# Kernel optimization log

Measured on AMD Instinct MI355X. Metric: run time of the kernel, lower is better.

The kernel has to match this reference:

```python
import jax, jax.numpy as jnp
import numpy as np

NSLICES = 4
HID = 512
IN_FEAT = 342   # input_shape - 1 (last column is phase)
OUT = 311
BATCH = 256


def cubic(y0, y1, y2, y3, mu):
    # Catmull-Rom cubic interpolation, as in the original PFNN code
    return (
        (-0.5 * y0 + 1.5 * y1 - 1.5 * y2 + 0.5 * y3) * mu * mu * mu
        + (y0 - 2.5 * y1 + 2.0 * y2 - 0.5 * y3) * mu * mu
        + (-0.5 * y0 + 0.5 * y2) * mu
        + y1
    )


def setup_inputs() -> dict:
    key = jax.random.key(0)
    ks = jax.random.split(key, 7)
    x = jax.random.uniform(ks[0], (BATCH, IN_FEAT + 1), dtype=jnp.float32)
    s = 0.02
    W0 = jax.random.normal(ks[1], (NSLICES, HID, IN_FEAT), dtype=jnp.float32) * s
    b0 = jax.random.normal(ks[2], (NSLICES, HID), dtype=jnp.float32) * s
    W1 = jax.random.normal(ks[3], (NSLICES, HID, HID), dtype=jnp.float32) * s
    b1 = jax.random.normal(ks[4], (NSLICES, HID), dtype=jnp.float32) * s
    W2 = jax.random.normal(ks[5], (NSLICES, OUT, HID), dtype=jnp.float32) * s
    b2 = jax.random.normal(ks[6], (NSLICES, OUT), dtype=jnp.float32) * s
    return {"x": x, "W0": W0, "b0": b0, "W1": W1, "b1": b1, "W2": W2, "b2": b2}


def reference(x, W0, b0, W1, b1, W2, b2):
    phase = x[:, -1]                       # [B]
    pscale = NSLICES * phase
    mu = jnp.mod(pscale, 1.0)              # [B]
    i1 = jnp.floor(pscale).astype(jnp.int32) % NSLICES
    i0 = (i1 - 1) % NSLICES
    i2 = (i1 + 1) % NSLICES
    i3 = (i1 + 2) % NSLICES
    muW = mu[:, None, None]                # broadcast over (out, in)
    mub = mu[:, None]

    Wb0 = cubic(W0[i0], W0[i1], W0[i2], W0[i3], muW)   # [B, 512, 342]
    bb0 = cubic(b0[i0], b0[i1], b0[i2], b0[i3], mub)   # [B, 512]
    Wb1 = cubic(W1[i0], W1[i1], W1[i2], W1[i3], muW)   # [B, 512, 512]
    bb1 = cubic(b1[i0], b1[i1], b1[i2], b1[i3], mub)
    Wb2 = cubic(W2[i0], W2[i1], W2[i2], W2[i3], muW)   # [B, 311, 512]
    bb2 = cubic(b2[i0], b2[i1], b2[i2], b2[i3], mub)

    h = x[:, :-1]                                       # [B, 342]
    h = jax.nn.elu(jnp.einsum('boi,bi->bo', Wb0, h) + bb0)
    h = jax.nn.elu(jnp.einsum('boi,bi->bo', Wb1, h) + bb1)
    out = jnp.einsum('boi,bi->bo', Wb2, h) + bb2        # [B, 311]
    return out
```

## Files before the change

### kernel.cpp

```cpp
#include <hip/hip_runtime.h>
#include <math.h>

#define NSLICES 4
#define HID 512
#define IN_FEAT 342
#define OUTD 311
#define BATCH 256
#define KP0 352
#define MP2 320
#define XROW (IN_FEAT + 1)

typedef unsigned short u16;
typedef short bf16x8 __attribute__((ext_vector_type(8)));
typedef float f32x4 __attribute__((ext_vector_type(4)));

__device__ __forceinline__ u16 f2bf_rne(float v) {
    unsigned int x = __float_as_uint(v);
    unsigned int r = (x + 0x7fffu + ((x >> 16) & 1u)) >> 16;
    return (u16)r;
}
__device__ __forceinline__ float bf2f(u16 u) {
    return __uint_as_float(((unsigned int)u) << 16);
}

#define C0 (4 * 512 * 44)
#define C1 (4 * 512 * 64)
#define C2 (4 * 320 * 64)
#define CX (256 * 44)
#define PREP_TOT (C0 + C1 + C2 + CX + 256)

union U8 { u16 u[8]; uint4 v; };

__global__ __launch_bounds__(256) void prep_all(
    const float* __restrict__ x,
    const float* __restrict__ W0, const float* __restrict__ W1, const float* __restrict__ W2,
    u16* __restrict__ whi0, u16* __restrict__ wlo0,
    u16* __restrict__ whi1, u16* __restrict__ wlo1,
    u16* __restrict__ whi2, u16* __restrict__ wlo2,
    u16* __restrict__ h0hi, u16* __restrict__ h0lo,
    float* __restrict__ dcoef)
{
    int i = blockIdx.x * 256 + threadIdx.x;
    if (i >= PREP_TOT) return;

    if (i >= C0 + C1 + C2 + CX) {
        int b = i - (C0 + C1 + C2 + CX);
        float ps = 4.f * x[(size_t)b * XROW + IN_FEAT];
        float fl = floorf(ps);
        float mu = ps - fl;
        int i1 = ((int)fl) & 3;
        float mu2 = mu * mu, mu3 = mu2 * mu;
        float c0 = -0.5f * mu3 + mu2 - 0.5f * mu;
        float c1 = 1.5f * mu3 - 2.5f * mu2 + 1.0f;
        float c2 = -1.5f * mu3 + 2.0f * mu2 + 0.5f * mu;
        float c3 = 0.5f * mu3 - 0.5f * mu2;
        float d[4];
        d[(i1 + 3) & 3] = c0;
        d[i1]           = c1;
        d[(i1 + 1) & 3] = c2;
        d[(i1 + 2) & 3] = c3;
        *reinterpret_cast<float4*>(dcoef + b * 4) = make_float4(d[0], d[1], d[2], d[3]);
        return;
    }

    float src[8];
    u16* dhi; u16* dlo; size_t doff;
    if (i < C0) {
        int row = i / 44, c = i - row * 44;
        int k = c * 8;
#pragma unroll
        for (int j = 0; j < 8; j++) {
            int kk = k + j;
            src[j] = (kk < IN_FEAT) ? W0[(size_t)row * IN_FEAT + kk] : 0.f;
        }
        dhi = whi0; dlo = wlo0; doff = (size_t)row * KP0 + k;
    } else if (i < C0 + C1) {
        int l = i - C0;
        int row = l >> 6, c = l & 63;
        int k = c * 8;
        const float* p = W1 + (size_t)row * HID + k;
#pragma unroll
        for (int j = 0; j < 8; j++) src[j] = p[j];
        dhi = whi1; dlo = wlo1; doff = (size_t)row * HID + k;
    } else if (i < C0 + C1 + C2) {
        int l = i - C0 - C1;
        int row = l >> 6, c = l & 63;
        int k = c * 8;
        int s = row / 320, o = row - s * 320;
        if (o < OUTD) {
            const float* p = W2 + ((size_t)s * OUTD + o) * HID + k;
#pragma unroll
            for (int j = 0; j < 8; j++) src[j] = p[j];
        } else {
#pragma unroll
            for (int j = 0; j < 8; j++) src[j] = 0.f;
        }
        dhi = whi2; dlo = wlo2; doff = (size_t)row * HID + k;
    } else {
        int l = i - C0 - C1 - C2;
        int b = l / 44, c = l - b * 44;
        int k = c * 8;
#pragma unroll
        for (int j = 0; j < 8; j++) {
            int kk = k + j;
            src[j] = (kk < IN_FEAT) ? x[(size_t)b * XROW + kk] : 0.f;
        }
        dhi = h0hi; dlo = h0lo; doff = (size_t)b * KP0 + k;
    }

    U8 hi, lo;
#pragma unroll
    for (int j = 0; j < 8; j++) {
        u16 h = f2bf_rne(src[j]);
        hi.u[j] = h;
        lo.u[j] = f2bf_rne(src[j] - bf2f(h));
    }
    *reinterpret_cast<uint4*>(dhi + doff) = hi.v;
    *reinterpret_cast<uint4*>(dlo + doff) = lo.v;
}

template<int KP, int KLDS, int FINAL>
__global__ __launch_bounds__(256, 2) void layer_fused2(
    const u16* __restrict__ Whi, const u16* __restrict__ Wlo,
    const u16* __restrict__ Hhi, const u16* __restrict__ Hlo,
    const float* __restrict__ bias, const float* __restrict__ dcoef,
    int Mp, int M,
    u16* __restrict__ Ohi, u16* __restrict__ Olo, float* __restrict__ out)
{
    __shared__ __align__(16) u16 sHhi[16 * KLDS];
    __shared__ __align__(16) u16 sHlo[16 * KLDS];
    __shared__ float sAcc[4][16][17];

    const int tid = (int)threadIdx.x;
    const int b0 = blockIdx.x * 16;
    const int o0 = blockIdx.y * 16;

    constexpr int CH = KP / 8;
    for (int idx = tid; idx < 16 * CH; idx += 256) {
        int r = idx / CH, c = idx - r * CH;
        size_t g = (size_t)(b0 + r) * KP + c * 8;
        *reinterpret_cast<uint4*>(&sHhi[r * KLDS + c * 8]) =
            *reinterpret_cast<const uint4*>(Hhi + g);
        *reinterpret_cast<uint4*>(&sHlo[r * KLDS + c * 8]) =
            *reinterpret_cast<const uint4*>(Hlo + g);
    }
    __syncthreads();

    const int lane = tid & 63;
    const int s  = tid >> 6;
    const int m  = lane & 15;
    const int q  = lane >> 4;

    const u16* hp_hi = &sHhi[m * KLDS + q * 8];
    const u16* hp_lo = &sHlo[m * KLDS + q * 8];
    const size_t wrow = ((size_t)s * Mp + o0 + m) * KP + q * 8;
    const u16* wp_hi = Whi + wrow;
    const u16* wp_lo = Wlo + wrow;

    f32x4 a0 = {0.f, 0.f, 0.f, 0.f};
    f32x4 a1 = {0.f, 0.f, 0.f, 0.f};
    f32x4 a2 = {0.f, 0.f, 0.f, 0.f};
#pragma unroll
    for (int c = 0; c < KP / 32; ++c) {
        bf16x8 ah = *reinterpret_cast<const bf16x8*>(wp_hi + c * 32);
        bf16x8 al = *reinterpret_cast<const bf16x8*>(wp_lo + c * 32);
        bf16x8 bh = *reinterpret_cast<const bf16x8*>(hp_hi + c * 32);
        bf16x8 b_l = *reinterpret_cast<const bf16x8*>(hp_lo + c * 32);
        a0 = __builtin_amdgcn_mfma_f32_16x16x32_bf16(ah, bh, a0, 0, 0, 0);
        a1 = __builtin_amdgcn_mfma_f32_16x16x32_bf16(ah, b_l, a1, 0, 0, 0);
        a2 = __builtin_amdgcn_mfma_f32_16x16x32_bf16(al, bh, a2, 0, 0, 0);
    }
    f32x4 sum = a0 + a1 + a2;

    const float ds = dcoef[(size_t)(b0 + m) * 4 + s];
#pragma unroll
    for (int r = 0; r < 4; ++r) {
        int o = o0 + q * 4 + r;
        float bb = (o < M) ? bias[(size_t)s * M + o] : 0.f;
        sAcc[s][q * 4 + r][m] = ds * (sum[r] + bb);
    }
    __syncthreads();

    const int o_l = tid & 15;
    const int b_l = tid >> 4;
    float v = sAcc[0][o_l][b_l] + sAcc[1][o_l][b_l]
            + sAcc[2][o_l][b_l] + sAcc[3][o_l][b_l];
    const int o = o0 + o_l;
    const int b = b0 + b_l;
    if (!FINAL) {
        float e = (v > 0.f) ? v : expm1f(v);
        u16 h = f2bf_rne(e);
        Ohi[(size_t)b * M + o] = h;
        Olo[(size_t)b * M + o] = f2bf_rne(e - bf2f(h));
    } else {
        if (o < M) out[(size_t)b * M + o] = v;
    }
}

extern "C" void kernel_launch(void* const* d_in, const int* in_sizes, int n_in,
                              void* d_out, int out_size, void* d_ws, size_t ws_size,
                              hipStream_t stream) {
    const float* x  = (const float*)d_in[0];
    const float* W0 = (const float*)d_in[1];
    const float* b0 = (const float*)d_in[2];
    const float* W1 = (const float*)d_in[3];
    const float* b1 = (const float*)d_in[4];
    const float* W2 = (const float*)d_in[5];
    const float* b2 = (const float*)d_in[6];
    float* out = (float*)d_out;

    char* p = (char*)d_ws;
    auto alloc = [&](size_t bytes) { char* r = p; p += (bytes + 255) & ~(size_t)255; return r; };

    float* dcoef = (float*)alloc(BATCH * 4 * sizeof(float));
    u16* whi0 = (u16*)alloc((size_t)4 * HID * KP0 * 2);
    u16* wlo0 = (u16*)alloc((size_t)4 * HID * KP0 * 2);
    u16* whi1 = (u16*)alloc((size_t)4 * HID * HID * 2);
    u16* wlo1 = (u16*)alloc((size_t)4 * HID * HID * 2);
    u16* whi2 = (u16*)alloc((size_t)4 * MP2 * HID * 2);
    u16* wlo2 = (u16*)alloc((size_t)4 * MP2 * HID * 2);
    u16* h0hi = (u16*)alloc((size_t)BATCH * KP0 * 2);
    u16* h0lo = (u16*)alloc((size_t)BATCH * KP0 * 2);
    u16* hahi = (u16*)alloc((size_t)BATCH * HID * 2);
    u16* halo = (u16*)alloc((size_t)BATCH * HID * 2);
    u16* hbhi = (u16*)alloc((size_t)BATCH * HID * 2);
    u16* hblo = (u16*)alloc((size_t)BATCH * HID * 2);

    prep_all<<<dim3((PREP_TOT + 255) / 256), 256, 0, stream>>>(
        x, W0, W1, W2, whi0, wlo0, whi1, wlo1, whi2, wlo2, h0hi, h0lo, dcoef);

    layer_fused2<KP0, KP0 + 8, 0><<<dim3(BATCH / 16, HID / 16), 256, 0, stream>>>(
        whi0, wlo0, h0hi, h0lo, b0, dcoef, HID, HID, hahi, halo, nullptr);

    layer_fused2<HID, HID + 8, 0><<<dim3(BATCH / 16, HID / 16), 256, 0, stream>>>(
        whi1, wlo1, hahi, halo, b1, dcoef, HID, HID, hbhi, hblo, nullptr);

    layer_fused2<HID, HID + 8, 1><<<dim3(BATCH / 16, MP2 / 16), 256, 0, stream>>>(
        whi2, wlo2, hbhi, hblo, b2, dcoef, MP2, OUTD, nullptr, nullptr, out);
}
```

Before: 102.2 us.

## Merge prep and three layers into one cooperative persistent kernel with grid syncs

Replaces four separate launches with a single cooperative kernel of 256 blocks that runs weight and activation splitting, then the three layers, with grid-wide syncs between phases. Each block now computes a 32-batch by 16-output tile, staging activations through LDS in chunks of 8 k-steps, so every weight fragment load feeds two MFMA batch tiles. This removes launch gaps and halves weight reloads per batch. In exchange it pays grid-sync overhead, gives less parallelism per layer (256 blocks, and only 160 active in the last layer), and adds extra block syncs for the chunked LDS staging.

```diff
diff --git a/kernel.cpp b/kernel.cpp
--- a/kernel.cpp
+++ b/kernel.cpp
@@ -1,7 +1,9 @@
 #include <hip/hip_runtime.h>
+#include <hip/hip_cooperative_groups.h>
 #include <math.h>
 
-#define NSLICES 4
+namespace cg = cooperative_groups;
+
 #define HID 512
 #define IN_FEAT 342
 #define OUTD 311
@@ -9,6 +11,7 @@
 #define KP0 352
 #define MP2 320
 #define XROW (IN_FEAT + 1)
+#define LSTRIDE 264
 
 typedef unsigned short u16;
 typedef short bf16x8 __attribute__((ext_vector_type(8)));
@@ -31,210 +34,237 @@
 
 union U8 { u16 u[8]; uint4 v; };
 
-__global__ __launch_bounds__(256) void prep_all(
-    const float* __restrict__ x,
-    const float* __restrict__ W0, const float* __restrict__ W1, const float* __restrict__ W2,
-    u16* __restrict__ whi0, u16* __restrict__ wlo0,
-    u16* __restrict__ whi1, u16* __restrict__ wlo1,
-    u16* __restrict__ whi2, u16* __restrict__ wlo2,
-    u16* __restrict__ h0hi, u16* __restrict__ h0lo,
-    float* __restrict__ dcoef)
+union SharedU {
+    u16 h[2][32 * LSTRIDE];
+    float acc[4][32][17];
+};
+
+struct Params {
+    const float *x, *W0, *b0, *W1, *b1, *W2, *b2;
+    float* out;
+    u16 *whi0, *wlo0, *whi1, *wlo1, *whi2, *wlo2;
+    u16 *h0hi, *h0lo, *hahi, *halo, *hbhi, *hblo;
+    float* dcoef;
+};
+
+__device__ __forceinline__ void layer_phase(
+    SharedU& sm,
+    const u16* __restrict__ Whi, const u16* __restrict__ Wlo, int wstride, int Mp,
+    const u16* __restrict__ Hhi, const u16* __restrict__ Hlo, int hstride, int nch,
+    const float* __restrict__ bias, const float* __restrict__ dcoef, int Mb,
+    int OT, int FINAL,
+    u16* __restrict__ Ohi, u16* __restrict__ Olo, float* __restrict__ outp)
 {
-    int i = blockIdx.x * 256 + threadIdx.x;
-    if (i >= PREP_TOT) return;
-
-    if (i >= C0 + C1 + C2 + CX) {
-        int b = i - (C0 + C1 + C2 + CX);
-        float ps = 4.f * x[(size_t)b * XROW + IN_FEAT];
-        float fl = floorf(ps);
-        float mu = ps - fl;
-        int i1 = ((int)fl) & 3;
-        float mu2 = mu * mu, mu3 = mu2 * mu;
-        float c0 = -0.5f * mu3 + mu2 - 0.5f * mu;
-        float c1 = 1.5f * mu3 - 2.5f * mu2 + 1.0f;
-        float c2 = -1.5f * mu3 + 2.0f * mu2 + 0.5f * mu;
-        float c3 = 0.5f * mu3 - 0.5f * mu2;
-        float d[4];
-        d[(i1 + 3) & 3] = c0;
-        d[i1]           = c1;
-        d[(i1 + 1) & 3] = c2;
-        d[(i1 + 2) & 3] = c3;
-        *reinterpret_cast<float4*>(dcoef + b * 4) = make_float4(d[0], d[1], d[2], d[3]);
-        return;
-    }
-
-    float src[8];
-    u16* dhi; u16* dlo; size_t doff;
-    if (i < C0) {
-        int row = i / 44, c = i - row * 44;
-        int k = c * 8;
-#pragma unroll
-        for (int j = 0; j < 8; j++) {
-            int kk = k + j;
-            src[j] = (kk < IN_FEAT) ? W0[(size_t)row * IN_FEAT + kk] : 0.f;
-        }
-        dhi = whi0; dlo = wlo0; doff = (size_t)row * KP0 + k;
-    } else if (i < C0 + C1) {
-        int l = i - C0;
-        int row = l >> 6, c = l & 63;
-        int k = c * 8;
-        const float* p = W1 + (size_t)row * HID + k;
-#pragma unroll
-        for (int j = 0; j < 8; j++) src[j] = p[j];
-        dhi = whi1; dlo = wlo1; doff = (size_t)row * HID + k;
-    } else if (i < C0 + C1 + C2) {
-        int l = i - C0 - C1;
-        int row = l >> 6, c = l & 63;
-        int k = c * 8;
-        int s = row / 320, o = row - s * 320;
-        if (o < OUTD) {
-            const float* p = W2 + ((size_t)s * OUTD + o) * HID + k;
-#pragma unroll
-            for (int j = 0; j < 8; j++) src[j] = p[j];
-        } else {
-#pragma unroll
-            for (int j = 0; j < 8; j++) src[j] = 0.f;
-        }
-        dhi = whi2; dlo = wlo2; doff = (size_t)row * HID + k;
-    } else {
-        int l = i - C0 - C1 - C2;
-        int b = l / 44, c = l - b * 44;
-        int k = c * 8;
-#pragma unroll
-        for (int j = 0; j < 8; j++) {
-            int kk = k + j;
-            src[j] = (kk < IN_FEAT) ? x[(size_t)b * XROW + kk] : 0.f;
-        }
-        dhi = h0hi; dlo = h0lo; doff = (size_t)b * KP0 + k;
-    }
-
-    U8 hi, lo;
-#pragma unroll
-    for (int j = 0; j < 8; j++) {
-        u16 h = f2bf_rne(src[j]);
-        hi.u[j] = h;
-        lo.u[j] = f2bf_rne(src[j] - bf2f(h));
-    }
-    *reinterpret_cast<uint4*>(dhi + doff) = hi.v;
-    *reinterpret_cast<uint4*>(dlo + doff) = lo.v;
-}
-
-template<int KP, int KLDS, int FINAL>
-__global__ __launch_bounds__(256, 2) void layer_fused2(
-    const u16* __restrict__ Whi, const u16* __restrict__ Wlo,
-    const u16* __restrict__ Hhi, const u16* __restrict__ Hlo,
-    const float* __restrict__ bias, const float* __restrict__ dcoef,
-    int Mp, int M,
-    u16* __restrict__ Ohi, u16* __restrict__ Olo, float* __restrict__ out)
-{
-    __shared__ __align__(16) u16 sHhi[16 * KLDS];
-    __shared__ __align__(16) u16 sHlo[16 * KLDS];
-    __shared__ float sAcc[4][16][17];
-
+    const int unit = (int)blockIdx.x;
+    if (unit >= OT * 8) return;
+    int ot, bq;
+    if (OT == 32) { ot = unit & 31; bq = unit >> 5; }
+    else          { ot = unit % OT; bq = unit / OT; }
+    const int o0 = ot * 16;
+    const int b0 = bq * 32;
     const int tid = (int)threadIdx.x;
-    const int b0 = blockIdx.x * 16;
-    const int o0 = blockIdx.y * 16;
-
-    constexpr int CH = KP / 8;
-    for (int idx = tid; idx < 16 * CH; idx += 256) {
-        int r = idx / CH, c = idx - r * CH;
-        size_t g = (size_t)(b0 + r) * KP + c * 8;
-        *reinterpret_cast<uint4*>(&sHhi[r * KLDS + c * 8]) =
-            *reinterpret_cast<const uint4*>(Hhi + g);
-        *reinterpret_cast<uint4*>(&sHlo[r * KLDS + c * 8]) =
-            *reinterpret_cast<const uint4*>(Hlo + g);
+    const int lane = tid & 63;
+    const int s = tid >> 6;
+    const int m = lane & 15;
+    const int q = lane >> 4;
+
+    f32x4 a0[2], a1[2], a2[2];
+#pragma unroll
+    for (int bt = 0; bt < 2; ++bt) {
+        a0[bt] = (f32x4){0.f, 0.f, 0.f, 0.f};
+        a1[bt] = (f32x4){0.f, 0.f, 0.f, 0.f};
+        a2[bt] = (f32x4){0.f, 0.f, 0.f, 0.f};
+    }
+
+    const u16* wph = Whi + ((size_t)s * Mp + o0 + m) * wstride + q * 8;
+    const u16* wpl = Wlo + ((size_t)s * Mp + o0 + m) * wstride + q * 8;
+
+    for (int c0 = 0; c0 < nch; c0 += 8) {
+        const int rc = (nch - c0 < 8) ? (nch - c0) : 8;
+        __syncthreads();
+        const int tot = 32 * rc * 4;
+        for (int idx = tid; idx < tot; idx += 256) {
+            int r = idx / (rc * 4);
+            int c = idx - r * (rc * 4);
+            size_t g = (size_t)(b0 + r) * hstride + c0 * 32 + c * 8;
+            *reinterpret_cast<uint4*>(&sm.h[0][r * LSTRIDE + c * 8]) =
+                *reinterpret_cast<const uint4*>(Hhi + g);
+            *reinterpret_cast<uint4*>(&sm.h[1][r * LSTRIDE + c * 8]) =
+                *reinterpret_cast<const uint4*>(Hlo + g);
+        }
+        __syncthreads();
+        for (int cc = 0; cc < rc; ++cc) {
+            bf16x8 ah = *reinterpret_cast<const bf16x8*>(wph + (size_t)(c0 + cc) * 32);
+            bf16x8 al = *reinterpret_cast<const bf16x8*>(wpl + (size_t)(c0 + cc) * 32);
+#pragma unroll
+            for (int bt = 0; bt < 2; ++bt) {
+                const u16* base = &sm.h[0][(bt * 16 + m) * LSTRIDE + cc * 32 + q * 8];
+                bf16x8 bh = *reinterpret_cast<const bf16x8*>(base);
+                bf16x8 bl = *reinterpret_cast<const bf16x8*>(base + 32 * LSTRIDE);
+                a0[bt] = __builtin_amdgcn_mfma_f32_16x16x32_bf16(ah, bh, a0[bt], 0, 0, 0);
+                a1[bt] = __builtin_amdgcn_mfma_f32_16x16x32_bf16(ah, bl, a1[bt], 0, 0, 0);
+                a2[bt] = __builtin_amdgcn_mfma_f32_16x16x32_bf16(al, bh, a2[bt], 0, 0, 0);
+            }
+        }
     }
     __syncthreads();
 
-    const int lane = tid & 63;
-    const int s  = tid >> 6;
-    const int m  = lane & 15;
-    const int q  = lane >> 4;
-
-    const u16* hp_hi = &sHhi[m * KLDS + q * 8];
-    const u16* hp_lo = &sHlo[m * KLDS + q * 8];
-    const size_t wrow = ((size_t)s * Mp + o0 + m) * KP + q * 8;
-    const u16* wp_hi = Whi + wrow;
-    const u16* wp_lo = Wlo + wrow;
-
-    f32x4 a0 = {0.f, 0.f, 0.f, 0.f};
-    f32x4 a1 = {0.f, 0.f, 0.f, 0.f};
-    f32x4 a2 = {0.f, 0.f, 0.f, 0.f};
-#pragma unroll
-    for (int c = 0; c < KP / 32; ++c) {
-        bf16x8 ah = *reinterpret_cast<const bf16x8*>(wp_hi + c * 32);
-        bf16x8 al = *reinterpret_cast<const bf16x8*>(wp_lo + c * 32);
-        bf16x8 bh = *reinterpret_cast<const bf16x8*>(hp_hi + c * 32);
-        bf16x8 b_l = *reinterpret_cast<const bf16x8*>(hp_lo + c * 32);
-        a0 = __builtin_amdgcn_mfma_f32_16x16x32_bf16(ah, bh, a0, 0, 0, 0);
-        a1 = __builtin_amdgcn_mfma_f32_16x16x32_bf16(ah, b_l, a1, 0, 0, 0);
-        a2 = __builtin_amdgcn_mfma_f32_16x16x32_bf16(al, bh, a2, 0, 0, 0);
-    }
-    f32x4 sum = a0 + a1 + a2;
-
-    const float ds = dcoef[(size_t)(b0 + m) * 4 + s];
+    float bb[4];
 #pragma unroll
     for (int r = 0; r < 4; ++r) {
         int o = o0 + q * 4 + r;
-        float bb = (o < M) ? bias[(size_t)s * M + o] : 0.f;
-        sAcc[s][q * 4 + r][m] = ds * (sum[r] + bb);
+        bb[r] = (o < Mb) ? bias[(size_t)s * Mb + o] : 0.f;
+    }
+    const float ds0 = dcoef[(size_t)(b0 + m) * 4 + s];
+    const float ds1 = dcoef[(size_t)(b0 + 16 + m) * 4 + s];
+#pragma unroll
+    for (int bt = 0; bt < 2; ++bt) {
+        f32x4 sum = a0[bt] + a1[bt] + a2[bt];
+        const float dsv = bt ? ds1 : ds0;
+#pragma unroll
+        for (int r = 0; r < 4; ++r)
+            sm.acc[s][bt * 16 + m][q * 4 + r] = dsv * (sum[r] + bb[r]);
     }
     __syncthreads();
 
-    const int o_l = tid & 15;
-    const int b_l = tid >> 4;
-    float v = sAcc[0][o_l][b_l] + sAcc[1][o_l][b_l]
-            + sAcc[2][o_l][b_l] + sAcc[3][o_l][b_l];
-    const int o = o0 + o_l;
-    const int b = b0 + b_l;
-    if (!FINAL) {
-        float e = (v > 0.f) ? v : expm1f(v);
-        u16 h = f2bf_rne(e);
-        Ohi[(size_t)b * M + o] = h;
-        Olo[(size_t)b * M + o] = f2bf_rne(e - bf2f(h));
-    } else {
-        if (o < M) out[(size_t)b * M + o] = v;
-    }
+    for (int idx = tid; idx < 512; idx += 256) {
+        int b_l = idx >> 4, o_l = idx & 15;
+        float v = sm.acc[0][b_l][o_l] + sm.acc[1][b_l][o_l]
+                + sm.acc[2][b_l][o_l] + sm.acc[3][b_l][o_l];
+        int o = o0 + o_l, b = b0 + b_l;
+        if (!FINAL) {
+            float e = (v > 0.f) ? v : expm1f(v);
+            u16 h = f2bf_rne(e);
+            Ohi[(size_t)b * HID + o] = h;
+            Olo[(size_t)b * HID + o] = f2bf_rne(e - bf2f(h));
+        } else if (o < OUTD) {
+            outp[(size_t)b * OUTD + o] = v;
+        }
+    }
+}
+
+__global__ __launch_bounds__(256) void pfn_coop(Params p)
+{
+    __shared__ SharedU sm;
+    cg::grid_group grid = cg::this_grid();
+
+    for (int i = (int)blockIdx.x * 256 + (int)threadIdx.x; i < PREP_TOT; i += 256 * 256) {
+        if (i >= C0 + C1 + C2 + CX) {
+            int b = i - (C0 + C1 + C2 + CX);
+            float ps = 4.f * p.x[(size_t)b * XROW + IN_FEAT];
+            float fl = floorf(ps);
+            float mu = ps - fl;
+            int i1 = ((int)fl) & 3;
+            float mu2 = mu * mu, mu3 = mu2 * mu;
+            float c0 = -0.5f * mu3 + mu2 - 0.5f * mu;
+            float c1 = 1.5f * mu3 - 2.5f * mu2 + 1.0f;
+            float c2 = -1.5f * mu3 + 2.0f * mu2 + 0.5f * mu;
+            float c3 = 0.5f * mu3 - 0.5f * mu2;
+            float d[4];
+            d[(i1 + 3) & 3] = c0;
+            d[i1]           = c1;
+            d[(i1 + 1) & 3] = c2;
+            d[(i1 + 2) & 3] = c3;
+            *reinterpret_cast<float4*>(p.dcoef + b * 4) = make_float4(d[0], d[1], d[2], d[3]);
+            continue;
+        }
+        float src[8];
+        u16 *dhi, *dlo; size_t doff;
+        if (i < C0) {
+            int row = i / 44, c = i - row * 44;
+            int k = c * 8;
+#pragma unroll
+            for (int j = 0; j < 8; j++) {
+                int kk = k + j;
+                src[j] = (kk < IN_FEAT) ? p.W0[(size_t)row * IN_FEAT + kk] : 0.f;
+            }
+            dhi = p.whi0; dlo = p.wlo0; doff = (size_t)row * KP0 + k;
+        } else if (i < C0 + C1) {
+            int l = i - C0;
+            int row = l >> 6, c = l & 63;
+            int k = c * 8;
+            const float* sp = p.W1 + (size_t)row * HID + k;
+#pragma unroll
+            for (int j = 0; j < 8; j++) src[j] = sp[j];
+            dhi = p.whi1; dlo = p.wlo1; doff = (size_t)row * HID + k;
+        } else if (i < C0 + C1 + C2) {
+            int l = i - C0 - C1;
+            int row = l >> 6, c = l & 63;
+            int k = c * 8;
+            int s = row / 320, o = row - s * 320;
+            if (o < OUTD) {
+                const float* sp = p.W2 + ((size_t)s * OUTD + o) * HID + k;
+#pragma unroll
+                for (int j = 0; j < 8; j++) src[j] = sp[j];
+            } else {
+#pragma unroll
+                for (int j = 0; j < 8; j++) src[j] = 0.f;
+            }
+            dhi = p.whi2; dlo = p.wlo2; doff = (size_t)row * HID + k;
+        } else {
+            int l = i - C0 - C1 - C2;
+            int b = l / 44, c = l - b * 44;
+            int k = c * 8;
+#pragma unroll
+            for (int j = 0; j < 8; j++) {
+                int kk = k + j;
+                src[j] = (kk < IN_FEAT) ? p.x[(size_t)b * XROW + kk] : 0.f;
+            }
+            dhi = p.h0hi; dlo = p.h0lo; doff = (size_t)b * KP0 + k;
+        }
+        U8 hi, lo;
+#pragma unroll
+        for (int j = 0; j < 8; j++) {
+            u16 h = f2bf_rne(src[j]);
+            hi.u[j] = h;
+            lo.u[j] = f2bf_rne(src[j] - bf2f(h));
+        }
+        *reinterpret_cast<uint4*>(dhi + doff) = hi.v;
+        *reinterpret_cast<uint4*>(dlo + doff) = lo.v;
+    }
+
+    grid.sync();
+    layer_phase(sm, p.whi0, p.wlo0, KP0, HID, p.h0hi, p.h0lo, KP0, 11,
+                p.b0, p.dcoef, HID, 32, 0, p.hahi, p.halo, nullptr);
+    grid.sync();
+    layer_phase(sm, p.whi1, p.wlo1, HID, HID, p.hahi, p.halo, HID, 16,
+                p.b1, p.dcoef, HID, 32, 0, p.hbhi, p.hblo, nullptr);
+    grid.sync();
+    layer_phase(sm, p.whi2, p.wlo2, HID, MP2, p.hbhi, p.hblo, HID, 16,
+                p.b2, p.dcoef, OUTD, 20, 1, nullptr, nullptr, p.out);
 }
 
 extern "C" void kernel_launch(void* const* d_in, const int* in_sizes, int n_in,
                               void* d_out, int out_size, void* d_ws, size_t ws_size,
                               hipStream_t stream) {
-    const float* x  = (const float*)d_in[0];
-    const float* W0 = (const float*)d_in[1];
-    const float* b0 = (const float*)d_in[2];
-    const float* W1 = (const float*)d_in[3];
-    const float* b1 = (const float*)d_in[4];
-    const float* W2 = (const float*)d_in[5];
-    const float* b2 = (const float*)d_in[6];
-    float* out = (float*)d_out;
-
-    char* p = (char*)d_ws;
-    auto alloc = [&](size_t bytes) { char* r = p; p += (bytes + 255) & ~(size_t)255; return r; };
-
-    float* dcoef = (float*)alloc(BATCH * 4 * sizeof(float));
-    u16* whi0 = (u16*)alloc((size_t)4 * HID * KP0 * 2);
-    u16* wlo0 = (u16*)alloc((size_t)4 * HID * KP0 * 2);
-    u16* whi1 = (u16*)alloc((size_t)4 * HID * HID * 2);
-    u16* wlo1 = (u16*)alloc((size_t)4 * HID * HID * 2);
-    u16* whi2 = (u16*)alloc((size_t)4 * MP2 * HID * 2);
-    u16* wlo2 = (u16*)alloc((size_t)4 * MP2 * HID * 2);
-    u16* h0hi = (u16*)alloc((size_t)BATCH * KP0 * 2);
-    u16* h0lo = (u16*)alloc((size_t)BATCH * KP0 * 2);
-    u16* hahi = (u16*)alloc((size_t)BATCH * HID * 2);
-    u16* halo = (u16*)alloc((size_t)BATCH * HID * 2);
-    u16* hbhi = (u16*)alloc((size_t)BATCH * HID * 2);
-    u16* hblo = (u16*)alloc((size_t)BATCH * HID * 2);
-
-    prep_all<<<dim3((PREP_TOT + 255) / 256), 256, 0, stream>>>(
-        x, W0, W1, W2, whi0, wlo0, whi1, wlo1, whi2, wlo2, h0hi, h0lo, dcoef);
-
-    layer_fused2<KP0, KP0 + 8, 0><<<dim3(BATCH / 16, HID / 16), 256, 0, stream>>>(
-        whi0, wlo0, h0hi, h0lo, b0, dcoef, HID, HID, hahi, halo, nullptr);
-
-    layer_fused2<HID, HID + 8, 0><<<dim3(BATCH / 16, HID / 16), 256, 0, stream>>>(
-        whi1, wlo1, hahi, halo, b1, dcoef, HID, HID, hbhi, hblo, nullptr);
-
-    layer_fused2<HID, HID + 8, 1><<<dim3(BATCH / 16, MP2 / 16), 256, 0, stream>>>(
-        whi2, wlo2, hbhi, hblo, b2, dcoef, MP2, OUTD, nullptr, nullptr, out);
-}
+    char* pw = (char*)d_ws;
+    auto alloc = [&](size_t bytes) { char* r = pw; pw += (bytes + 255) & ~(size_t)255; return r; };
+
+    Params p;
+    p.x  = (const float*)d_in[0];
+    p.W0 = (const float*)d_in[1];
+    p.b0 = (const float*)d_in[2];
+    p.W1 = (const float*)d_in[3];
+    p.b1 = (const float*)d_in[4];
+    p.W2 = (const float*)d_in[5];
+    p.b2 = (const float*)d_in[6];
+    p.out = (float*)d_out;
+
+    p.dcoef = (float*)alloc(BATCH * 4 * sizeof(float));
+    p.whi0 = (u16*)alloc((size_t)4 * HID * KP0 * 2);
+    p.wlo0 = (u16*)alloc((size_t)4 * HID * KP0 * 2);
+    p.whi1 = (u16*)alloc((size_t)4 * HID * HID * 2);
+    p.wlo1 = (u16*)alloc((size_t)4 * HID * HID * 2);
+    p.whi2 = (u16*)alloc((size_t)4 * MP2 * HID * 2);
+    p.wlo2 = (u16*)alloc((size_t)4 * MP2 * HID * 2);
+    p.h0hi = (u16*)alloc((size_t)BATCH * KP0 * 2);
+    p.h0lo = (u16*)alloc((size_t)BATCH * KP0 * 2);
+    p.hahi = (u16*)alloc((size_t)BATCH * HID * 2);
+    p.halo = (u16*)alloc((size_t)BATCH * HID * 2);
+    p.hbhi = (u16*)alloc((size_t)BATCH * HID * 2);
+    p.hblo = (u16*)alloc((size_t)BATCH * HID * 2);
+
+    void* args[] = { &p };
+    hipLaunchCooperativeKernel(reinterpret_cast<const void*>(&pfn_coop),
+                               dim3(256), dim3(256), args, 0, stream);
+}
```

Result: slower. 214.8 us (+110.2%).

## Fuse weight bf16 split conversion into layer kernels, drop prep pass

Applied to the files above, without the earlier changes.

Removes the separate prep kernel that converted all weights and inputs into hi/lo bf16 arrays in workspace. Each layer kernel now reads fp32 weights directly and splits them into hi/lo bf16 in registers before the MFMAs. Layer 0 converts x in shared memory, and every kernel computes its own blend coefficients. This saves a launch and a write-then-read round trip of the converted weights. In exchange, each weight row is now read as fp32 (twice the bytes) by every batch tile and reconverted there, and shared memory is unioned between the activations and the accumulator.

```diff
diff --git a/kernel.cpp b/kernel.cpp
--- a/kernel.cpp
+++ b/kernel.cpp
@@ -1,14 +1,12 @@
 #include <hip/hip_runtime.h>
 #include <math.h>
 
-#define NSLICES 4
 #define HID 512
 #define IN_FEAT 342
 #define OUTD 311
 #define BATCH 256
+#define XROW (IN_FEAT + 1)
 #define KP0 352
-#define MP2 320
-#define XROW (IN_FEAT + 1)
 
 typedef unsigned short u16;
 typedef short bf16x8 __attribute__((ext_vector_type(8)));
@@ -23,29 +21,109 @@
     return __uint_as_float(((unsigned int)u) << 16);
 }
 
-#define C0 (4 * 512 * 44)
-#define C1 (4 * 512 * 64)
-#define C2 (4 * 320 * 64)
-#define CX (256 * 44)
-#define PREP_TOT (C0 + C1 + C2 + CX + 256)
+__device__ __forceinline__ void cvt8(const float* v, bf16x8& hi, bf16x8& lo) {
+#pragma unroll
+    for (int j = 0; j < 8; j++) {
+        unsigned int xu = __float_as_uint(v[j]);
+        unsigned int rnd = xu + 0x7fffu + ((xu >> 16) & 1u);
+        hi[j] = (short)(rnd >> 16);
+        float lof = v[j] - __uint_as_float(rnd & 0xffff0000u);
+        lo[j] = (short)(__float_as_uint(lof) >> 16);
+    }
+}
 
-union U8 { u16 u[8]; uint4 v; };
+template<int KCH, int KLDS, int FINAL, int L0>
+__global__ __launch_bounds__(256, 2) void layer_direct(
+    const float* __restrict__ W,
+    int Kw, int Mreal, int Mb,
+    const float* __restrict__ x,
+    const u16* __restrict__ Hhi, const u16* __restrict__ Hlo,
+    const float* __restrict__ bias,
+    u16* __restrict__ Ohi, u16* __restrict__ Olo, float* __restrict__ outp)
+{
+    union SharedU {
+        u16 h[2][16 * KLDS];
+        float acc[4][16][17];
+    };
+    __shared__ SharedU sm;
 
-__global__ __launch_bounds__(256) void prep_all(
-    const float* __restrict__ x,
-    const float* __restrict__ W0, const float* __restrict__ W1, const float* __restrict__ W2,
-    u16* __restrict__ whi0, u16* __restrict__ wlo0,
-    u16* __restrict__ whi1, u16* __restrict__ wlo1,
-    u16* __restrict__ whi2, u16* __restrict__ wlo2,
-    u16* __restrict__ h0hi, u16* __restrict__ h0lo,
-    float* __restrict__ dcoef)
-{
-    int i = blockIdx.x * 256 + threadIdx.x;
-    if (i >= PREP_TOT) return;
+    const int tid = (int)threadIdx.x;
+    const int b0 = (int)blockIdx.x * 16;
+    const int o0 = (int)blockIdx.y * 16;
 
-    if (i >= C0 + C1 + C2 + CX) {
-        int b = i - (C0 + C1 + C2 + CX);
-        float ps = 4.f * x[(size_t)b * XROW + IN_FEAT];
+    if (L0) {
+        for (int idx = tid; idx < 16 * KP0; idx += 256) {
+            int r = idx / KP0, k = idx - r * KP0;
+            float v = (k < IN_FEAT) ? x[(size_t)(b0 + r) * XROW + k] : 0.f;
+            u16 h = f2bf_rne(v);
+            sm.h[0][r * KLDS + k] = h;
+            sm.h[1][r * KLDS + k] = f2bf_rne(v - bf2f(h));
+        }
+    } else {
+        constexpr int CH = KCH * 4;
+        for (int idx = tid; idx < 16 * CH; idx += 256) {
+            int r = idx / CH, c = idx - r * CH;
+            size_t g = (size_t)(b0 + r) * HID + c * 8;
+            *reinterpret_cast<uint4*>(&sm.h[0][r * KLDS + c * 8]) =
+                *reinterpret_cast<const uint4*>(Hhi + g);
+            *reinterpret_cast<uint4*>(&sm.h[1][r * KLDS + c * 8]) =
+                *reinterpret_cast<const uint4*>(Hlo + g);
+        }
+    }
+    __syncthreads();
+
+    const int lane = tid & 63;
+    const int s = tid >> 6;
+    const int m = lane & 15;
+    const int q = lane >> 4;
+
+    int orow = o0 + m;
+    if (orow >= Mreal) orow = Mreal - 1;
+    const float* wr = W + ((size_t)s * Mreal + orow) * Kw;
+
+    const u16* hp = &sm.h[0][m * KLDS + q * 8];
+
+    f32x4 a0 = {0.f, 0.f, 0.f, 0.f};
+    f32x4 a1 = {0.f, 0.f, 0.f, 0.f};
+    f32x4 a2 = {0.f, 0.f, 0.f, 0.f};
+
+#pragma unroll
+    for (int cc = 0; cc < KCH; ++cc) {
+        const int kb = cc * 32 + q * 8;
+        float v[8];
+        if (L0) {
+            if (cc < KCH - 1) {
+#pragma unroll
+                for (int t = 0; t < 4; t++) {
+                    float2 f2 = *reinterpret_cast<const float2*>(wr + kb + t * 2);
+                    v[t * 2] = f2.x; v[t * 2 + 1] = f2.y;
+                }
+            } else {
+#pragma unroll
+                for (int j = 0; j < 8; j++) {
+                    int k = kb + j;
+                    v[j] = (k < IN_FEAT) ? wr[k] : 0.f;
+                }
+            }
+        } else {
+            float4 f4a = *reinterpret_cast<const float4*>(wr + kb);
+            float4 f4b = *reinterpret_cast<const float4*>(wr + kb + 4);
+            v[0] = f4a.x; v[1] = f4a.y; v[2] = f4a.z; v[3] = f4a.w;
+            v[4] = f4b.x; v[5] = f4b.y; v[6] = f4b.z; v[7] = f4b.w;
+        }
+        bf16x8 ah, al;
+        cvt8(v, ah, al);
+        bf16x8 bh = *reinterpret_cast<const bf16x8*>(hp + cc * 32);
+        bf16x8 bl = *reinterpret_cast<const bf16x8*>(hp + cc * 32 + 16 * KLDS);
+        a0 = __builtin_amdgcn_mfma_f32_16x16x32_bf16(ah, bh, a0, 0, 0, 0);
+        a1 = __builtin_amdgcn_mfma_f32_16x16x32_bf16(ah, bl, a1, 0, 0, 0);
+        a2 = __builtin_amdgcn_mfma_f32_16x16x32_bf16(al, bh, a2, 0, 0, 0);
+    }
+    __syncthreads();
+
+    float ds;
+    {
+        float ps = 4.f * x[(size_t)(b0 + m) * XROW + IN_FEAT];
         float fl = floorf(ps);
         float mu = ps - fl;
         int i1 = ((int)fl) & 3;
@@ -54,146 +132,32 @@
         float c1 = 1.5f * mu3 - 2.5f * mu2 + 1.0f;
         float c2 = -1.5f * mu3 + 2.0f * mu2 + 0.5f * mu;
         float c3 = 0.5f * mu3 - 0.5f * mu2;
-        float d[4];
-        d[(i1 + 3) & 3] = c0;
-        d[i1]           = c1;
-        d[(i1 + 1) & 3] = c2;
-        d[(i1 + 2) & 3] = c3;
-        *reinterpret_cast<float4*>(dcoef + b * 4) = make_float4(d[0], d[1], d[2], d[3]);
-        return;
+        int k = (s + 1 - i1) & 3;
+        ds = (k == 0) ? c0 : (k == 1) ? c1 : (k == 2) ? c2 : c3;
     }
 
-    float src[8];
-    u16* dhi; u16* dlo; size_t doff;
-    if (i < C0) {
-        int row = i / 44, c = i - row * 44;
-        int k = c * 8;
-#pragma unroll
-        for (int j = 0; j < 8; j++) {
-            int kk = k + j;
-            src[j] = (kk < IN_FEAT) ? W0[(size_t)row * IN_FEAT + kk] : 0.f;
-        }
-        dhi = whi0; dlo = wlo0; doff = (size_t)row * KP0 + k;
-    } else if (i < C0 + C1) {
-        int l = i - C0;
-        int row = l >> 6, c = l & 63;
-        int k = c * 8;
-        const float* p = W1 + (size_t)row * HID + k;
-#pragma unroll
-        for (int j = 0; j < 8; j++) src[j] = p[j];
-        dhi = whi1; dlo = wlo1; doff = (size_t)row * HID + k;
-    } else if (i < C0 + C1 + C2) {
-        int l = i - C0 - C1;
-        int row = l >> 6, c = l & 63;
-        int k = c * 8;
-        int s = row / 320, o = row - s * 320;
-        if (o < OUTD) {
-            const float* p = W2 + ((size_t)s * OUTD + o) * HID + k;
-#pragma unroll
-            for (int j = 0; j < 8; j++) src[j] = p[j];
-        } else {
-#pragma unroll
-            for (int j = 0; j < 8; j++) src[j] = 0.f;
-        }
-        dhi = whi2; dlo = wlo2; doff = (size_t)row * HID + k;
-    } else {
-        int l = i - C0 - C1 - C2;
-        int b = l / 44, c = l - b * 44;
-        int k = c * 8;
-#pragma unroll
-        for (int j = 0; j < 8; j++) {
-            int kk = k + j;
-            src[j] = (kk < IN_FEAT) ? x[(size_t)b * XROW + kk] : 0.f;
-        }
-        dhi = h0hi; dlo = h0lo; doff = (size_t)b * KP0 + k;
-    }
-
-    U8 hi, lo;
-#pragma unroll
-    for (int j = 0; j < 8; j++) {
-        u16 h = f2bf_rne(src[j]);
-        hi.u[j] = h;
-        lo.u[j] = f2bf_rne(src[j] - bf2f(h));
-    }
-    *reinterpret_cast<uint4*>(dhi + doff) = hi.v;
-    *reinterpret_cast<uint4*>(dlo + doff) = lo.v;
-}
-
-template<int KP, int KLDS, int FINAL>
-__global__ __launch_bounds__(256, 2) void layer_fused2(
-    const u16* __restrict__ Whi, const u16* __restrict__ Wlo,
-    const u16* __restrict__ Hhi, const u16* __restrict__ Hlo,
-    const float* __restrict__ bias, const float* __restrict__ dcoef,
-    int Mp, int M,
-    u16* __restrict__ Ohi, u16* __restrict__ Olo, float* __restrict__ out)
-{
-    __shared__ __align__(16) u16 sHhi[16 * KLDS];
-    __shared__ __align__(16) u16 sHlo[16 * KLDS];
-    __shared__ float sAcc[4][16][17];
-
-    const int tid = (int)threadIdx.x;
-    const int b0 = blockIdx.x * 16;
-    const int o0 = blockIdx.y * 16;
-
-    constexpr int CH = KP / 8;
-    for (int idx = tid; idx < 16 * CH; idx += 256) {
-        int r = idx / CH, c = idx - r * CH;
-        size_t g = (size_t)(b0 + r) * KP + c * 8;
-        *reinterpret_cast<uint4*>(&sHhi[r * KLDS + c * 8]) =
-            *reinterpret_cast<const uint4*>(Hhi + g);
-        *reinterpret_cast<uint4*>(&sHlo[r * KLDS + c * 8]) =
-            *reinterpret_cast<const uint4*>(Hlo + g);
-    }
-    __syncthreads();
-
-    const int lane = tid & 63;
-    const int s  = tid >> 6;
-    const int m  = lane & 15;
-    const int q  = lane >> 4;
-
-    const u16* hp_hi = &sHhi[m * KLDS + q * 8];
-    const u16* hp_lo = &sHlo[m * KLDS + q * 8];
-    const size_t wrow = ((size_t)s * Mp + o0 + m) * KP + q * 8;
-    const u16* wp_hi = Whi + wrow;
-    const u16* wp_lo = Wlo + wrow;
-
-    f32x4 a0 = {0.f, 0.f, 0.f, 0.f};
-    f32x4 a1 = {0.f, 0.f, 0.f, 0.f};
-    f32x4 a2 = {0.f, 0.f, 0.f, 0.f};
-#pragma unroll
-    for (int c = 0; c < KP / 32; ++c) {
-        bf16x8 ah = *reinterpret_cast<const bf16x8*>(wp_hi + c * 32);
-        bf16x8 al = *reinterpret_cast<const bf16x8*>(wp_lo + c * 32);
-        bf16x8 bh = *reinterpret_cast<const bf16x8*>(hp_hi + c * 32);
-        bf16x8 b_l = *reinterpret_cast<const bf16x8*>(hp_lo + c * 32);
-        a0 = __builtin_amdgcn_mfma_f32_16x16x32_bf16(ah, bh, a0, 0, 0, 0);
-        a1 = __builtin_amdgcn_mfma_f32_16x16x32_bf16(ah, b_l, a1, 0, 0, 0);
-        a2 = __builtin_amdgcn_mfma_f32_16x16x32_bf16(al, bh, a2, 0, 0, 0);
-    }
     f32x4 sum = a0 + a1 + a2;
-
-    const float ds = dcoef[(size_t)(b0 + m) * 4 + s];
 #pragma unroll
     for (int r = 0; r < 4; ++r) {
         int o = o0 + q * 4 + r;
-        float bb = (o < M) ? bias[(size_t)s * M + o] : 0.f;
-        sAcc[s][q * 4 + r][m] = ds * (sum[r] + bb);
+        float bb = (o < Mb) ? bias[(size_t)s * Mb + o] : 0.f;
+        sm.acc[s][q * 4 + r][m] = ds * (sum[r] + bb);
     }
     __syncthreads();
 
     const int o_l = tid & 15;
     const int b_l = tid >> 4;
-    float v = sAcc[0][o_l][b_l] + sAcc[1][o_l][b_l]
-            + sAcc[2][o_l][b_l] + sAcc[3][o_l][b_l];
+    float vv = sm.acc[0][o_l][b_l] + sm.acc[1][o_l][b_l]
+             + sm.acc[2][o_l][b_l] + sm.acc[3][o_l][b_l];
     const int o = o0 + o_l;
     const int b = b0 + b_l;
     if (!FINAL) {
-        float e = (v > 0.f) ? v : expm1f(v);
+        float e = (vv > 0.f) ? vv : expm1f(vv);
         u16 h = f2bf_rne(e);
-        Ohi[(size_t)b * M + o] = h;
-        Olo[(size_t)b * M + o] = f2bf_rne(e - bf2f(h));
-    } else {
-        if (o < M) out[(size_t)b * M + o] = v;
+        Ohi[(size_t)b * HID + o] = h;
+        Olo[(size_t)b * HID + o] = f2bf_rne(e - bf2f(h));
+    } else if (o < OUTD) {
+        outp[(size_t)b * OUTD + o] = vv;
     }
 }
 
@@ -209,32 +173,19 @@
     const float* b2 = (const float*)d_in[6];
     float* out = (float*)d_out;
 
-    char* p = (char*)d_ws;
-    auto alloc = [&](size_t bytes) { char* r = p; p += (bytes + 255) & ~(size_t)255; return r; };
-
-    float* dcoef = (float*)alloc(BATCH * 4 * sizeof(float));
-    u16* whi0 = (u16*)alloc((size_t)4 * HID * KP0 * 2);
-    u16* wlo0 = (u16*)alloc((size_t)4 * HID * KP0 * 2);
-    u16* whi1 = (u16*)alloc((size_t)4 * HID * HID * 2);
-    u16* wlo1 = (u16*)alloc((size_t)4 * HID * HID * 2);
-    u16* whi2 = (u16*)alloc((size_t)4 * MP2 * HID * 2);
-    u16* wlo2 = (u16*)alloc((size_t)4 * MP2 * HID * 2);
-    u16* h0hi = (u16*)alloc((size_t)BATCH * KP0 * 2);
-    u16* h0lo = (u16*)alloc((size_t)BATCH * KP0 * 2);
+    char* pw = (char*)d_ws;
+    auto alloc = [&](size_t bytes) { char* r = pw; pw += (bytes + 255) & ~(size_t)255; return r; };
     u16* hahi = (u16*)alloc((size_t)BATCH * HID * 2);
     u16* halo = (u16*)alloc((size_t)BATCH * HID * 2);
     u16* hbhi = (u16*)alloc((size_t)BATCH * HID * 2);
     u16* hblo = (u16*)alloc((size_t)BATCH * HID * 2);
 
-    prep_all<<<dim3((PREP_TOT + 255) / 256), 256, 0, stream>>>(
-        x, W0, W1, W2, whi0, wlo0, whi1, wlo1, whi2, wlo2, h0hi, h0lo, dcoef);
+    layer_direct<11, 360, 0, 1><<<dim3(BATCH / 16, HID / 16), 256, 0, stream>>>(
+        W0, IN_FEAT, HID, HID, x, nullptr, nullptr, b0, hahi, halo, nullptr);
 
-    layer_fused2<KP0, KP0 + 8, 0><<<dim3(BATCH / 16, HID / 16), 256, 0, stream>>>(
-        whi0, wlo0, h0hi, h0lo, b0, dcoef, HID, HID, hahi, halo, nullptr);
+    layer_direct<16, 520, 0, 0><<<dim3(BATCH / 16, HID / 16), 256, 0, stream>>>(
+        W1, HID, HID, HID, x, hahi, halo, b1, hbhi, hblo, nullptr);
 
-    layer_fused2<HID, HID + 8, 0><<<dim3(BATCH / 16, HID / 16), 256, 0, stream>>>(
-        whi1, wlo1, hahi, halo, b1, dcoef, HID, HID, hbhi, hblo, nullptr);
-
-    layer_fused2<HID, HID + 8, 1><<<dim3(BATCH / 16, MP2 / 16), 256, 0, stream>>>(
-        whi2, wlo2, hbhi, hblo, b2, dcoef, MP2, OUTD, nullptr, nullptr, out);
+    layer_direct<16, 520, 1, 0><<<dim3(BATCH / 16, 20), 256, 0, stream>>>(
+        W2, HID, OUTD, OUTD, x, hbhi, hblo, b2, nullptr, nullptr, out);
 }
```

Measured after the change: 105.5 us. +3.3%, slower.

## Widen batch tile to 32 rows for hidden layers, reuse weight loads across two waves

Applied to the files above, without the earlier changes.

The layer kernel is templated on batch tile size NB. The first two layers now use 32 batch rows per block with 512 threads, so each slice's weight fragment serves two 16-row batch groups and the block count halves. The LDS activation buffers and the reduction buffer now share a union, which requires an extra barrier after the MFMA loop. The trade-off is fewer blocks (8x32) and occupancy hint 1, and each wave still loads its weights from global memory separately, so any reuse depends on cache hits.

```diff
diff --git a/kernel.cpp b/kernel.cpp
--- a/kernel.cpp
+++ b/kernel.cpp
@@ -1,7 +1,6 @@
 #include <hip/hip_runtime.h>
 #include <math.h>
 
-#define NSLICES 4
 #define HID 512
 #define IN_FEAT 342
 #define OUTD 311
@@ -64,7 +63,7 @@
     }
 
     float src[8];
-    u16* dhi; u16* dlo; size_t doff;
+    u16 *dhi, *dlo; size_t doff;
     if (i < C0) {
         int row = i / 44, c = i - row * 44;
         int k = c * 8;
@@ -119,81 +118,85 @@
     *reinterpret_cast<uint4*>(dlo + doff) = lo.v;
 }
 
-template<int KP, int KLDS, int FINAL>
-__global__ __launch_bounds__(256, 2) void layer_fused2(
-    const u16* __restrict__ Whi, const u16* __restrict__ Wlo,
+template<int KP, int KLDS, int NB, int FINAL>
+__global__ __launch_bounds__(NB * 16, (NB == 16 ? 2 : 1)) void layer_v3(
+    const u16* __restrict__ Whi, const u16* __restrict__ Wlo, int Mp,
     const u16* __restrict__ Hhi, const u16* __restrict__ Hlo,
-    const float* __restrict__ bias, const float* __restrict__ dcoef,
-    int Mp, int M,
-    u16* __restrict__ Ohi, u16* __restrict__ Olo, float* __restrict__ out)
+    const float* __restrict__ bias, const float* __restrict__ dcoef, int Mb,
+    u16* __restrict__ Ohi, u16* __restrict__ Olo, float* __restrict__ outp)
 {
-    __shared__ __align__(16) u16 sHhi[16 * KLDS];
-    __shared__ __align__(16) u16 sHlo[16 * KLDS];
-    __shared__ float sAcc[4][16][17];
+    union SharedU {
+        u16 h[2][NB * KLDS];
+        float acc[4][NB][17];
+    };
+    __shared__ SharedU sm;
 
     const int tid = (int)threadIdx.x;
-    const int b0 = blockIdx.x * 16;
-    const int o0 = blockIdx.y * 16;
+    const int b0 = (int)blockIdx.x * NB;
+    const int o0 = (int)blockIdx.y * 16;
+    constexpr int NTHR = NB * 16;
 
     constexpr int CH = KP / 8;
-    for (int idx = tid; idx < 16 * CH; idx += 256) {
+    for (int idx = tid; idx < NB * CH; idx += NTHR) {
         int r = idx / CH, c = idx - r * CH;
         size_t g = (size_t)(b0 + r) * KP + c * 8;
-        *reinterpret_cast<uint4*>(&sHhi[r * KLDS + c * 8]) =
+        *reinterpret_cast<uint4*>(&sm.h[0][r * KLDS + c * 8]) =
             *reinterpret_cast<const uint4*>(Hhi + g);
-        *reinterpret_cast<uint4*>(&sHlo[r * KLDS + c * 8]) =
+        *reinterpret_cast<uint4*>(&sm.h[1][r * KLDS + c * 8]) =
             *reinterpret_cast<const uint4*>(Hlo + g);
     }
     __syncthreads();
 
     const int lane = tid & 63;
-    const int s  = tid >> 6;
-    const int m  = lane & 15;
-    const int q  = lane >> 4;
-
-    const u16* hp_hi = &sHhi[m * KLDS + q * 8];
-    const u16* hp_lo = &sHlo[m * KLDS + q * 8];
-    const size_t wrow = ((size_t)s * Mp + o0 + m) * KP + q * 8;
-    const u16* wp_hi = Whi + wrow;
-    const u16* wp_lo = Wlo + wrow;
+    const int w = tid >> 6;
+    const int s = w & 3;
+    const int t = w >> 2;
+    const int m = lane & 15;
+    const int q = lane >> 4;
+
+    const size_t wro = ((size_t)s * Mp + o0 + m) * KP + q * 8;
+    const u16* wph = Whi + wro;
+    const u16* wpl = Wlo + wro;
+    const u16* hp = &sm.h[0][(t * 16 + m) * KLDS + q * 8];
 
     f32x4 a0 = {0.f, 0.f, 0.f, 0.f};
     f32x4 a1 = {0.f, 0.f, 0.f, 0.f};
     f32x4 a2 = {0.f, 0.f, 0.f, 0.f};
 #pragma unroll
-    for (int c = 0; c < KP / 32; ++c) {
-        bf16x8 ah = *reinterpret_cast<const bf16x8*>(wp_hi + c * 32);
-        bf16x8 al = *reinterpret_cast<const bf16x8*>(wp_lo + c * 32);
-        bf16x8 bh = *reinterpret_cast<const bf16x8*>(hp_hi + c * 32);
-        bf16x8 b_l = *reinterpret_cast<const bf16x8*>(hp_lo + c * 32);
+    for (int cc = 0; cc < KP / 32; ++cc) {
+        bf16x8 ah = *reinterpret_cast<const bf16x8*>(wph + cc * 32);
+        bf16x8 al = *reinterpret_cast<const bf16x8*>(wpl + cc * 32);
+        bf16x8 bh = *reinterpret_cast<const bf16x8*>(hp + cc * 32);
+        bf16x8 bl = *reinterpret_cast<const bf16x8*>(hp + cc * 32 + NB * KLDS);
         a0 = __builtin_amdgcn_mfma_f32_16x16x32_bf16(ah, bh, a0, 0, 0, 0);
-        a1 = __builtin_amdgcn_mfma_f32_16x16x32_bf16(ah, b_l, a1, 0, 0, 0);
+        a1 = __builtin_amdgcn_mfma_f32_16x16x32_bf16(ah, bl, a1, 0, 0, 0);
         a2 = __builtin_amdgcn_mfma_f32_16x16x32_bf16(al, bh, a2, 0, 0, 0);
     }
+    __syncthreads();
+
+    const float ds = dcoef[(size_t)(b0 + t * 16 + m) * 4 + s];
     f32x4 sum = a0 + a1 + a2;
-
-    const float ds = dcoef[(size_t)(b0 + m) * 4 + s];
 #pragma unroll
     for (int r = 0; r < 4; ++r) {
         int o = o0 + q * 4 + r;
-        float bb = (o < M) ? bias[(size_t)s * M + o] : 0.f;
-        sAcc[s][q * 4 + r][m] = ds * (sum[r] + bb);
+        float bb = (o < Mb) ? bias[(size_t)s * Mb + o] : 0.f;
+        sm.acc[s][t * 16 + m][q * 4 + r] = ds * (sum[r] + bb);
     }
     __syncthreads();
 
+    const int b_l = tid >> 4;
     const int o_l = tid & 15;
-    const int b_l = tid >> 4;
-    float v = sAcc[0][o_l][b_l] + sAcc[1][o_l][b_l]
-            + sAcc[2][o_l][b_l] + sAcc[3][o_l][b_l];
+    float vv = sm.acc[0][b_l][o_l] + sm.acc[1][b_l][o_l]
+             + sm.acc[2][b_l][o_l] + sm.acc[3][b_l][o_l];
     const int o = o0 + o_l;
     const int b = b0 + b_l;
     if (!FINAL) {
-        float e = (v > 0.f) ? v : expm1f(v);
+        float e = (vv > 0.f) ? vv : expm1f(vv);
         u16 h = f2bf_rne(e);
-        Ohi[(size_t)b * M + o] = h;
-        Olo[(size_t)b * M + o] = f2bf_rne(e - bf2f(h));
-    } else {
-        if (o < M) out[(size_t)b * M + o] = v;
+        Ohi[(size_t)b * HID + o] = h;
+        Olo[(size_t)b * HID + o] = f2bf_rne(e - bf2f(h));
+    } else if (o < OUTD) {
+        outp[(size_t)b * OUTD + o] = vv;
     }
 }
 
@@ -209,8 +212,8 @@
     const float* b2 = (const float*)d_in[6];
     float* out = (float*)d_out;
 
-    char* p = (char*)d_ws;
-    auto alloc = [&](size_t bytes) { char* r = p; p += (bytes + 255) & ~(size_t)255; return r; };
+    char* pw = (char*)d_ws;
+    auto alloc = [&](size_t bytes) { char* r = pw; pw += (bytes + 255) & ~(size_t)255; return r; };
 
     float* dcoef = (float*)alloc(BATCH * 4 * sizeof(float));
     u16* whi0 = (u16*)alloc((size_t)4 * HID * KP0 * 2);
@@ -229,12 +232,12 @@
     prep_all<<<dim3((PREP_TOT + 255) / 256), 256, 0, stream>>>(
         x, W0, W1, W2, whi0, wlo0, whi1, wlo1, whi2, wlo2, h0hi, h0lo, dcoef);
 
-    layer_fused2<KP0, KP0 + 8, 0><<<dim3(BATCH / 16, HID / 16), 256, 0, stream>>>(
-        whi0, wlo0, h0hi, h0lo, b0, dcoef, HID, HID, hahi, halo, nullptr);
-
-    layer_fused2<HID, HID + 8, 0><<<dim3(BATCH / 16, HID / 16), 256, 0, stream>>>(
-        whi1, wlo1, hahi, halo, b1, dcoef, HID, HID, hbhi, hblo, nullptr);
-
-    layer_fused2<HID, HID + 8, 1><<<dim3(BATCH / 16, MP2 / 16), 256, 0, stream>>>(
-        whi2, wlo2, hbhi, hblo, b2, dcoef, MP2, OUTD, nullptr, nullptr, out);
-}
+    layer_v3<KP0, 360, 32, 0><<<dim3(BATCH / 32, HID / 16), 512, 0, stream>>>(
+        whi0, wlo0, HID, h0hi, h0lo, b0, dcoef, HID, hahi, halo, nullptr);
+
+    layer_v3<HID, 520, 32, 0><<<dim3(BATCH / 32, HID / 16), 512, 0, stream>>>(
+        whi1, wlo1, HID, hahi, halo, b1, dcoef, HID, hbhi, hblo, nullptr);
+
+    layer_v3<HID, 520, 16, 1><<<dim3(BATCH / 16, MP2 / 16), 256, 0, stream>>>(
+        whi2, wlo2, MP2, hbhi, hblo, b2, dcoef, OUTD, nullptr, nullptr, out);
+}
```

Result: no change. 102.1 us (-0.0%).
